# Optimization experiments

Hardware: AMD Instinct MI355X
Metric: run time of the kernel (lower is better)

Reference implementation:

```python
import jax, jax.numpy as jnp
import numpy as np

WML, B, S, D = 64, 64, 40, 512  # word_max_len, batch, sents_max_len, dim


def setup_inputs() -> dict:
    key = jax.random.key(0)
    ks = jax.random.split(key, 8)
    source = jax.random.normal(ks[0], (B, D), dtype=jnp.float32)
    word_bank = jax.random.normal(ks[1], (WML, B, S, D), dtype=jnp.float32)
    # per-sentence word counts in [1, WML] so every sentence has >=1 valid token
    word_lengths = jax.random.randint(ks[2], (B, S), 1, WML + 1)
    sent_bank = jax.random.normal(ks[3], (S, B, D), dtype=jnp.float32)
    sent_lengths = jax.random.randint(ks[4], (B,), 1, S + 1)  # unused by forward math
    static_attn = jax.random.uniform(ks[5], (B, S), dtype=jnp.float32)
    scale = 1.0 / np.sqrt(D)
    W_word = jax.random.normal(ks[6], (D, D), dtype=jnp.float32) * scale
    W_sent = jax.random.normal(ks[7], (D, D), dtype=jnp.float32) * scale
    W_out = jax.random.normal(jax.random.fold_in(key, 99), (D, 2 * D), dtype=jnp.float32) * scale
    return {"source": source, "word_bank": word_bank, "word_lengths": word_lengths,
            "sent_bank": sent_bank, "sent_lengths": sent_lengths, "static_attn": static_attn,
            "W_word": W_word, "W_sent": W_sent, "W_out": W_out}


def reference(source, word_bank, word_lengths, sent_bank, sent_lengths, static_attn, W_word, W_sent, W_out):
    wml, batch, sents, dim = word_bank.shape
    # [wml, B, S, D] -> [B, S, wml, D] -> [B, S*wml, D]  (matches torch transpose chain)
    wb = jnp.transpose(word_bank, (1, 2, 0, 3)).reshape(batch, sents * wml, dim)
    # score(source, wb, 'word'): (source @ W_word^T) dotted with each word vector
    word_align = jnp.einsum('bd,bnd->bn', source @ W_word.T, wb)          # [B, S*wml]
    sb = jnp.transpose(sent_bank, (1, 0, 2))                               # [B, S, D]
    sent_align = jnp.einsum('bd,bsd->bs', source @ W_sent.T, sb)          # [B, S]
    # triple product: word score * sentence score * static attention
    align = (word_align.reshape(batch, sents, wml)
             * (sent_align * static_attn)[:, :, None]).reshape(batch, sents * wml)
    # sequence mask per sentence, flattened to [B, S*wml]
    mask = (jnp.arange(wml)[None, None, :] < word_lengths[:, :, None]).reshape(batch, sents * wml)
    align = jnp.where(mask, align, -jnp.inf)
    align_vectors = jax.nn.softmax(align, axis=-1) + 1e-20               # [B, S*wml]
    c = jnp.einsum('bn,bnd->bd', align_vectors, wb)                       # [B, D]
    attn_h = jnp.tanh(jnp.concatenate([c, source], axis=-1) @ W_out.T)    # [B, D]
    return attn_h, align_vectors
```

## Files before the change

### kernel.cpp

```cpp
#include <hip/hip_runtime.h>
#include <math.h>

#define BB   64
#define SS   40
#define WMLC 64
#define DD   512
#define NN   2560
#define NBLK 20
#define WPB  4
#define NWAVES (NBLK*WPB)
#define RPW (NN/NWAVES)
#define ABLK (NN/256)
#define L2E 1.4426950408889634f

__device__ __forceinline__ float wave_reduce_sum(float v) {
    #pragma unroll
    for (int off = 32; off > 0; off >>= 1) v += __shfl_xor(v, off, 64);
    return v;
}

__global__ __launch_bounds__(256) void k_proj(const float* __restrict__ src,
                                              const float* __restrict__ Ww,
                                              const float* __restrict__ Ws,
                                              const float* __restrict__ sb,
                                              const float* __restrict__ sa,
                                              float* __restrict__ qw,
                                              float* __restrict__ sstat) {
    __shared__ float xs[DD];
    __shared__ float qsl[DD];
    const int b = blockIdx.y;
    const int t = threadIdx.x;
    const bool sent = blockIdx.x != 0;
    const float* W = sent ? Ws : Ww;
    ((float2*)xs)[t] = ((const float2*)(src + b * DD))[t];
    __syncthreads();
    const float* r0 = W + (size_t)t * DD;
    const float* r1 = W + (size_t)(t + 256) * DD;
    float acc0 = 0.f, acc1 = 0.f;
    for (int k = 0; k < DD; k += 4) {
        float4 x  = *(const float4*)(xs + k);
        float4 w0 = *(const float4*)(r0 + k);
        float4 w1 = *(const float4*)(r1 + k);
        acc0 += x.x * w0.x + x.y * w0.y + x.z * w0.z + x.w * w0.w;
        acc1 += x.x * w1.x + x.y * w1.y + x.z * w1.z + x.w * w1.w;
    }
    if (!sent) {
        qw[b * DD + t] = acc0;
        qw[b * DD + t + 256] = acc1;
        return;
    }
    qsl[t] = acc0;
    qsl[t + 256] = acc1;
    __syncthreads();
    const int wave = t >> 6, lane = t & 63;
    const int d0 = lane * 4, d1 = 256 + lane * 4;
    const float4 q0 = *(const float4*)(qsl + d0);
    const float4 q1 = *(const float4*)(qsl + d1);
    for (int j = 0; j < SS / WPB; ++j) {
        const int s = wave * (SS / WPB) + j;
        const float* row = sb + ((size_t)s * BB + b) * DD;
        float4 a0 = *(const float4*)(row + d0);
        float4 a1 = *(const float4*)(row + d1);
        float p = a0.x * q0.x + a0.y * q0.y + a0.z * q0.z + a0.w * q0.w
                + a1.x * q1.x + a1.y * q1.y + a1.z * q1.z + a1.w * q1.w;
        p = wave_reduce_sum(p);
        if (lane == 0) sstat[b * SS + s] = p * sa[b * SS + s];
    }
}

#define PROCESS_ROW()                                                          \
    {                                                                          \
        float p = p0.x * qa0.x + p0.y * qa0.y + p0.z * qa0.z + p0.w * qa0.w    \
                + p1.x * qa1.x + p1.y * qa1.y + p1.z * qa1.z + p1.w * qa1.w;   \
        p = wave_reduce_sum(p);                                                \
        const float a = p * s_st[pn >> 6];                                     \
        if (lane == 0) scores[b * NN + pn] = a;                                \
        if (a > m) {                                                           \
            const float sc = (m == -INFINITY) ? 0.f : exp2f((m - a) * L2E);    \
            l *= sc;                                                           \
            c0.x *= sc; c0.y *= sc; c0.z *= sc; c0.w *= sc;                    \
            c1.x *= sc; c1.y *= sc; c1.z *= sc; c1.w *= sc;                    \
            m = a;                                                             \
        }                                                                      \
        const float e = exp2f((a - m) * L2E);                                  \
        l += e;                                                                \
        c0.x += e * p0.x; c0.y += e * p0.y; c0.z += e * p0.z; c0.w += e * p0.w;\
        c1.x += e * p1.x; c1.y += e * p1.y; c1.z += e * p1.z; c1.w += e * p1.w;\
    }

__global__ __launch_bounds__(256) void k_main(const float* __restrict__ wb,
                                              const float* __restrict__ qw,
                                              const float* __restrict__ sstat,
                                              const int* __restrict__ wl,
                                              float* __restrict__ scores,
                                              float* __restrict__ part_c,
                                              float* __restrict__ part_ml) {
    __shared__ int   s_wl[SS];
    __shared__ float s_st[SS];
    __shared__ float s_m[WPB], s_l[WPB];
    __shared__ float s_c[WPB][DD];
    const int b = blockIdx.y;
    const int chunk = blockIdx.x;
    const int t = threadIdx.x, wave = t >> 6, lane = t & 63;
    if (t < SS) {
        s_wl[t] = wl[b * SS + t];
        s_st[t] = sstat[b * SS + t];
    }
    const int gw = chunk * WPB + wave;
    const int d0 = lane * 4, d1 = 256 + lane * 4;
    const float4 qa0 = *(const float4*)(qw + b * DD + d0);
    const float4 qa1 = *(const float4*)(qw + b * DD + d1);
    __syncthreads();

    float m = -INFINITY, l = 0.f;
    float4 c0 = {0.f, 0.f, 0.f, 0.f}, c1 = {0.f, 0.f, 0.f, 0.f};

    int    pn = -1;
    float4 p0 = {0.f, 0.f, 0.f, 0.f}, p1 = {0.f, 0.f, 0.f, 0.f};

    int k = 0;
    for (; k < RPW; ++k) {
        const int n = gw + k * NWAVES;
        const int s = n >> 6, w = n & 63;
        if (w < s_wl[s]) {
            const float* row = wb + (size_t)((w * BB + b) * SS + s) * DD;
            p0 = *(const float4*)(row + d0);
            p1 = *(const float4*)(row + d1);
            pn = n;
            ++k;
            break;
        }
    }
    for (; k < RPW; ++k) {
        const int n = gw + k * NWAVES;
        const int s = n >> 6, w = n & 63;
        if (w >= s_wl[s]) continue;
        const float* row = wb + (size_t)((w * BB + b) * SS + s) * DD;
        const float4 f0 = *(const float4*)(row + d0);
        const float4 f1 = *(const float4*)(row + d1);
        PROCESS_ROW();
        p0 = f0; p1 = f1; pn = n;
    }
    if (pn >= 0) PROCESS_ROW();

    *(float4*)(&s_c[wave][d0]) = c0;
    *(float4*)(&s_c[wave][d1]) = c1;
    if (lane == 0) { s_m[wave] = m; s_l[wave] = l; }
    __syncthreads();
    const float mb = fmaxf(fmaxf(s_m[0], s_m[1]), fmaxf(s_m[2], s_m[3]));
    float lb = 0.f, cA = 0.f, cB = 0.f;
    #pragma unroll
    for (int wv = 0; wv < WPB; ++wv) {
        const float mi = s_m[wv];
        const float sc = (mi == -INFINITY) ? 0.f : exp2f((mi - mb) * L2E);
        lb += s_l[wv] * sc;
        cA += s_c[wv][t] * sc;
        cB += s_c[wv][t + 256] * sc;
    }
    const int pidx = b * NBLK + chunk;
    part_c[(size_t)pidx * DD + t] = cA;
    part_c[(size_t)pidx * DD + t + 256] = cB;
    if (t == 0) { part_ml[pidx * 2] = mb; part_ml[pidx * 2 + 1] = lb; }
}

__global__ __launch_bounds__(256) void k_reduce(const float* __restrict__ part_c,
                                                const float* __restrict__ part_ml,
                                                float* __restrict__ c_final,
                                                float* __restrict__ mz) {
    const int b = blockIdx.x, t = threadIdx.x;
    float mg = -INFINITY;
    for (int i = 0; i < NBLK; ++i) mg = fmaxf(mg, part_ml[(b * NBLK + i) * 2]);
    float Z = 0.f, cA = 0.f, cB = 0.f;
    for (int i = 0; i < NBLK; ++i) {
        const float mi = part_ml[(b * NBLK + i) * 2];
        const float li = part_ml[(b * NBLK + i) * 2 + 1];
        const float sc = (mi == -INFINITY) ? 0.f : exp2f((mi - mg) * L2E);
        Z += li * sc;
        cA += part_c[(size_t)(b * NBLK + i) * DD + t] * sc;
        cB += part_c[(size_t)(b * NBLK + i) * DD + t + 256] * sc;
    }
    const float invZ = 1.0f / Z;
    c_final[b * DD + t] = cA * invZ;
    c_final[b * DD + t + 256] = cB * invZ;
    if (t == 0) { mz[b * 2] = mg; mz[b * 2 + 1] = invZ; }
}

__global__ __launch_bounds__(256) void k_fin(const int* __restrict__ wl,
                                             const float* __restrict__ mz,
                                             float* __restrict__ av,
                                             const float* __restrict__ c_final,
                                             const float* __restrict__ src,
                                             const float* __restrict__ Wout,
                                             float* __restrict__ out) {
    __shared__ float xs[2 * DD];
    const int b = blockIdx.y;
    const int t = threadIdx.x;
    if (blockIdx.x < ABLK) {
        const int n = blockIdx.x * 256 + t;
        const int s = n >> 6, w = n & 63;
        const int len = wl[b * SS + s];
        float v = 1e-20f;
        if (w < len) {
            const float a = av[b * NN + n];
            v = exp2f((a - mz[b * 2]) * L2E) * mz[b * 2 + 1] + 1e-20f;
        }
        av[b * NN + n] = v;
        return;
    }
    ((float2*)xs)[t] = ((const float2*)(c_final + b * DD))[t];
    ((float2*)(xs + DD))[t] = ((const float2*)(src + b * DD))[t];
    __syncthreads();
    const int d = (blockIdx.x - ABLK) * 256 + t;
    const float* row = Wout + (size_t)d * (2 * DD);
    float acc = 0.f;
    for (int k = 0; k < 2 * DD; k += 4) {
        float4 x = *(const float4*)(xs + k);
        float4 w = *(const float4*)(row + k);
        acc += x.x * w.x + x.y * w.y + x.z * w.z + x.w * w.w;
    }
    out[b * DD + d] = tanhf(acc);
}

extern "C" void kernel_launch(void* const* d_in, const int* in_sizes, int n_in,
                              void* d_out, int out_size, void* d_ws, size_t ws_size,
                              hipStream_t stream) {
    const float* src = (const float*)d_in[0];
    const float* wb  = (const float*)d_in[1];
    const int*   wl  = (const int*)  d_in[2];
    const float* sb  = (const float*)d_in[3];
    const float* sa  = (const float*)d_in[5];
    const float* Ww  = (const float*)d_in[6];
    const float* Wsn = (const float*)d_in[7];
    const float* Wo  = (const float*)d_in[8];
    float* out = (float*)d_out;

    float* ws = (float*)d_ws;
    float* qw      = ws;
    float* sstat   = ws + 32768;
    float* part_c  = ws + 35328;
    float* part_ml = ws + 690688;
    float* mz      = ws + 693248;
    float* c_final = ws + 693376;

    float* scores = out + BB * DD;

    hipLaunchKernelGGL(k_proj,   dim3(2, BB),        dim3(256), 0, stream,
                       src, Ww, Wsn, sb, sa, qw, sstat);
    hipLaunchKernelGGL(k_main,   dim3(NBLK, BB),     dim3(256), 0, stream,
                       wb, qw, sstat, wl, scores, part_c, part_ml);
    hipLaunchKernelGGL(k_reduce, dim3(BB),           dim3(256), 0, stream,
                       part_c, part_ml, c_final, mz);
    hipLaunchKernelGGL(k_fin,    dim3(ABLK + 2, BB), dim3(256), 0, stream,
                       wl, mz, scores, c_final, src, Wo, out);
}
```

Baseline: 513.5 us.

## Split projection GEMVs across more blocks and fold reduce kernel into final kernel

The projection kernel now uses 8 blocks per batch row instead of 2. Threads split each output row across lane pairs, and the sentence scores are written as four partial sums that k_main adds together and multiplies by static attention. The separate reduce kernel is removed: every k_fin block recomputes the global max and normaliser from the per-chunk partials, and the output GEMV blocks also merge the partial context vectors. The output projection uses 64 rows per block across 8 blocks with a 4-way lane split. This cuts a launch and raises parallelism in the small GEMVs, at the cost of redundant max/sum work in every k_fin block.

```diff
diff --git a/kernel.cpp b/kernel.cpp
--- a/kernel.cpp
+++ b/kernel.cpp
@@ -11,6 +11,7 @@
 #define NWAVES (NBLK*WPB)
 #define RPW (NN/NWAVES)
 #define ABLK (NN/256)
+#define HBLK 8
 #define L2E 1.4426950408889634f
 
 __device__ __forceinline__ float wave_reduce_sum(float v) {
@@ -23,48 +24,46 @@
                                               const float* __restrict__ Ww,
                                               const float* __restrict__ Ws,
                                               const float* __restrict__ sb,
-                                              const float* __restrict__ sa,
                                               float* __restrict__ qw,
-                                              float* __restrict__ sstat) {
+                                              float* __restrict__ sstat_part) {
     __shared__ float xs[DD];
-    __shared__ float qsl[DD];
+    __shared__ float qsl[128];
     const int b = blockIdx.y;
     const int t = threadIdx.x;
-    const bool sent = blockIdx.x != 0;
+    const bool sent = blockIdx.x >= 4;
+    const int chunk = sent ? (blockIdx.x - 4) : blockIdx.x;
     const float* W = sent ? Ws : Ww;
     ((float2*)xs)[t] = ((const float2*)(src + b * DD))[t];
     __syncthreads();
-    const float* r0 = W + (size_t)t * DD;
-    const float* r1 = W + (size_t)(t + 256) * DD;
-    float acc0 = 0.f, acc1 = 0.f;
-    for (int k = 0; k < DD; k += 4) {
-        float4 x  = *(const float4*)(xs + k);
-        float4 w0 = *(const float4*)(r0 + k);
-        float4 w1 = *(const float4*)(r1 + k);
-        acc0 += x.x * w0.x + x.y * w0.y + x.z * w0.z + x.w * w0.w;
-        acc1 += x.x * w1.x + x.y * w1.y + x.z * w1.z + x.w * w1.w;
-    }
+
+    const int j = t >> 1, half = t & 1;
+    const int d = chunk * 128 + j;
+    const float* r = W + (size_t)d * DD + half * 256;
+    const float* x = xs + half * 256;
+    float acc = 0.f;
+    for (int k = 0; k < 256; k += 4) {
+        float4 xv = *(const float4*)(x + k);
+        float4 wv = *(const float4*)(r + k);
+        acc += xv.x * wv.x + xv.y * wv.y + xv.z * wv.z + xv.w * wv.w;
+    }
+    acc += __shfl_xor(acc, 1, 64);
+
     if (!sent) {
-        qw[b * DD + t] = acc0;
-        qw[b * DD + t + 256] = acc1;
+        if (half == 0) qw[b * DD + d] = acc;
         return;
     }
-    qsl[t] = acc0;
-    qsl[t + 256] = acc1;
-    __syncthreads();
+    if (half == 0) qsl[j] = acc;
+    __syncthreads();
+
     const int wave = t >> 6, lane = t & 63;
-    const int d0 = lane * 4, d1 = 256 + lane * 4;
-    const float4 q0 = *(const float4*)(qsl + d0);
-    const float4 q1 = *(const float4*)(qsl + d1);
-    for (int j = 0; j < SS / WPB; ++j) {
-        const int s = wave * (SS / WPB) + j;
-        const float* row = sb + ((size_t)s * BB + b) * DD;
-        float4 a0 = *(const float4*)(row + d0);
-        float4 a1 = *(const float4*)(row + d1);
-        float p = a0.x * q0.x + a0.y * q0.y + a0.z * q0.z + a0.w * q0.w
-                + a1.x * q1.x + a1.y * q1.y + a1.z * q1.z + a1.w * q1.w;
+    const float2 q = *(const float2*)(qsl + lane * 2);
+    for (int jj = 0; jj < SS / WPB; ++jj) {
+        const int s = wave * (SS / WPB) + jj;
+        const float* row = sb + ((size_t)s * BB + b) * DD + chunk * 128;
+        float2 a = *(const float2*)(row + lane * 2);
+        float p = a.x * q.x + a.y * q.y;
         p = wave_reduce_sum(p);
-        if (lane == 0) sstat[b * SS + s] = p * sa[b * SS + s];
+        if (lane == 0) sstat_part[(b * SS + s) * 4 + chunk] = p;
     }
 }
 
@@ -90,7 +89,8 @@
 
 __global__ __launch_bounds__(256) void k_main(const float* __restrict__ wb,
                                               const float* __restrict__ qw,
-                                              const float* __restrict__ sstat,
+                                              const float* __restrict__ sstat_part,
+                                              const float* __restrict__ sa,
                                               const int* __restrict__ wl,
                                               float* __restrict__ scores,
                                               float* __restrict__ part_c,
@@ -104,7 +104,8 @@
     const int t = threadIdx.x, wave = t >> 6, lane = t & 63;
     if (t < SS) {
         s_wl[t] = wl[b * SS + t];
-        s_st[t] = sstat[b * SS + t];
+        const float4 pp = *(const float4*)(sstat_part + (b * SS + t) * 4);
+        s_st[t] = (pp.x + pp.y + pp.z + pp.w) * sa[b * SS + t];
     }
     const int gw = chunk * WPB + wave;
     const int d0 = lane * 4, d1 = 256 + lane * 4;
@@ -163,38 +164,32 @@
     if (t == 0) { part_ml[pidx * 2] = mb; part_ml[pidx * 2 + 1] = lb; }
 }
 
-__global__ __launch_bounds__(256) void k_reduce(const float* __restrict__ part_c,
-                                                const float* __restrict__ part_ml,
-                                                float* __restrict__ c_final,
-                                                float* __restrict__ mz) {
-    const int b = blockIdx.x, t = threadIdx.x;
-    float mg = -INFINITY;
-    for (int i = 0; i < NBLK; ++i) mg = fmaxf(mg, part_ml[(b * NBLK + i) * 2]);
-    float Z = 0.f, cA = 0.f, cB = 0.f;
-    for (int i = 0; i < NBLK; ++i) {
-        const float mi = part_ml[(b * NBLK + i) * 2];
-        const float li = part_ml[(b * NBLK + i) * 2 + 1];
-        const float sc = (mi == -INFINITY) ? 0.f : exp2f((mi - mg) * L2E);
-        Z += li * sc;
-        cA += part_c[(size_t)(b * NBLK + i) * DD + t] * sc;
-        cB += part_c[(size_t)(b * NBLK + i) * DD + t + 256] * sc;
-    }
-    const float invZ = 1.0f / Z;
-    c_final[b * DD + t] = cA * invZ;
-    c_final[b * DD + t + 256] = cB * invZ;
-    if (t == 0) { mz[b * 2] = mg; mz[b * 2 + 1] = invZ; }
-}
-
 __global__ __launch_bounds__(256) void k_fin(const int* __restrict__ wl,
-                                             const float* __restrict__ mz,
+                                             const float* __restrict__ part_c,
+                                             const float* __restrict__ part_ml,
                                              float* __restrict__ av,
-                                             const float* __restrict__ c_final,
                                              const float* __restrict__ src,
                                              const float* __restrict__ Wout,
                                              float* __restrict__ out) {
     __shared__ float xs[2 * DD];
     const int b = blockIdx.y;
     const int t = threadIdx.x;
+
+    float mg = -INFINITY;
+    #pragma unroll
+    for (int i = 0; i < NBLK; ++i)
+        mg = fmaxf(mg, part_ml[(b * NBLK + i) * 2]);
+    float Z = 0.f;
+    float sc[NBLK];
+    #pragma unroll
+    for (int i = 0; i < NBLK; ++i) {
+        const float mi = part_ml[(b * NBLK + i) * 2];
+        const float li = part_ml[(b * NBLK + i) * 2 + 1];
+        sc[i] = (mi == -INFINITY) ? 0.f : exp2f((mi - mg) * L2E);
+        Z += li * sc[i];
+    }
+    const float invZ = 1.0f / Z;
+
     if (blockIdx.x < ABLK) {
         const int n = blockIdx.x * 256 + t;
         const int s = n >> 6, w = n & 63;
@@ -202,23 +197,36 @@
         float v = 1e-20f;
         if (w < len) {
             const float a = av[b * NN + n];
-            v = exp2f((a - mz[b * 2]) * L2E) * mz[b * 2 + 1] + 1e-20f;
+            v = exp2f((a - mg) * L2E) * invZ + 1e-20f;
         }
         av[b * NN + n] = v;
         return;
     }
-    ((float2*)xs)[t] = ((const float2*)(c_final + b * DD))[t];
+
+    float cA = 0.f, cB = 0.f;
+    #pragma unroll
+    for (int i = 0; i < NBLK; ++i) {
+        cA += part_c[(size_t)(b * NBLK + i) * DD + t] * sc[i];
+        cB += part_c[(size_t)(b * NBLK + i) * DD + t + 256] * sc[i];
+    }
+    xs[t] = cA * invZ;
+    xs[t + 256] = cB * invZ;
     ((float2*)(xs + DD))[t] = ((const float2*)(src + b * DD))[t];
     __syncthreads();
-    const int d = (blockIdx.x - ABLK) * 256 + t;
-    const float* row = Wout + (size_t)d * (2 * DD);
+
+    const int j = t >> 2, quarter = t & 3;
+    const int d = (blockIdx.x - ABLK) * 64 + j;
+    const float* row = Wout + (size_t)d * (2 * DD) + quarter * 256;
+    const float* x = xs + quarter * 256;
     float acc = 0.f;
-    for (int k = 0; k < 2 * DD; k += 4) {
-        float4 x = *(const float4*)(xs + k);
-        float4 w = *(const float4*)(row + k);
-        acc += x.x * w.x + x.y * w.y + x.z * w.z + x.w * w.w;
-    }
-    out[b * DD + d] = tanhf(acc);
+    for (int k = 0; k < 256; k += 4) {
+        float4 xv = *(const float4*)(x + k);
+        float4 wv = *(const float4*)(row + k);
+        acc += xv.x * wv.x + xv.y * wv.y + xv.z * wv.z + xv.w * wv.w;
+    }
+    acc += __shfl_xor(acc, 1, 64);
+    acc += __shfl_xor(acc, 2, 64);
+    if (quarter == 0) out[b * DD + d] = tanhf(acc);
 }
 
 extern "C" void kernel_launch(void* const* d_in, const int* in_sizes, int n_in,
@@ -235,21 +243,17 @@
     float* out = (float*)d_out;
 
     float* ws = (float*)d_ws;
-    float* qw      = ws;
-    float* sstat   = ws + 32768;
-    float* part_c  = ws + 35328;
-    float* part_ml = ws + 690688;
-    float* mz      = ws + 693248;
-    float* c_final = ws + 693376;
+    float* qw         = ws;
+    float* sstat_part = ws + 32768;
+    float* part_c     = ws + 43008;
+    float* part_ml    = ws + 698368;
 
     float* scores = out + BB * DD;
 
-    hipLaunchKernelGGL(k_proj,   dim3(2, BB),        dim3(256), 0, stream,
-                       src, Ww, Wsn, sb, sa, qw, sstat);
-    hipLaunchKernelGGL(k_main,   dim3(NBLK, BB),     dim3(256), 0, stream,
-                       wb, qw, sstat, wl, scores, part_c, part_ml);
-    hipLaunchKernelGGL(k_reduce, dim3(BB),           dim3(256), 0, stream,
-                       part_c, part_ml, c_final, mz);
-    hipLaunchKernelGGL(k_fin,    dim3(ABLK + 2, BB), dim3(256), 0, stream,
-                       wl, mz, scores, c_final, src, Wo, out);
-}
+    hipLaunchKernelGGL(k_proj, dim3(8, BB),           dim3(256), 0, stream,
+                       src, Ww, Wsn, sb, qw, sstat_part);
+    hipLaunchKernelGGL(k_main, dim3(NBLK, BB),        dim3(256), 0, stream,
+                       wb, qw, sstat_part, sa, wl, scores, part_c, part_ml);
+    hipLaunchKernelGGL(k_fin,  dim3(ABLK + HBLK, BB), dim3(256), 0, stream,
+                       wl, part_c, part_ml, scores, src, Wo, out);
+}
```

Result: faster. 487.0 us (-5.2%).
